# Performance work log

Hardware: AMD Instinct MI355X
Metric: run time of the kernel (lower is better)

## Reference

```python
import jax, jax.numpy as jnp
import numpy as np

N_NODES = 50000
N_EDGES = 800000
D_IN = 128
D_HID = 256
N_CLASSES = 2
N_GRAPHS = 256


def _graph_conv(x, src, dst, W_root, W_rel, b, num_nodes):
    # PyG GraphConv: out_i = W_root @ x_i + W_rel @ sum_{j->i} x_j + b
    agg = jax.ops.segment_sum(x[src], dst, num_segments=num_nodes)  # [N, d_in]
    return x @ W_root.T + agg @ W_rel.T + b


def setup_inputs() -> dict:
    key = jax.random.key(0)
    ks = jax.random.split(key, 12)
    x = jax.random.normal(ks[0], (N_NODES, D_IN), dtype=jnp.float32)
    edge_index = jax.random.randint(ks[1], (2, N_EDGES), 0, N_NODES, dtype=jnp.int64)
    batch = jnp.sort(jax.random.randint(ks[2], (N_NODES,), 0, N_GRAPHS, dtype=jnp.int64))
    s1 = 1.0 / np.sqrt(D_IN)
    s2 = 1.0 / np.sqrt(D_HID)
    W1_root = jax.random.uniform(ks[3], (D_HID, D_IN), minval=-s1, maxval=s1, dtype=jnp.float32)
    W1_rel = jax.random.uniform(ks[4], (D_HID, D_IN), minval=-s1, maxval=s1, dtype=jnp.float32)
    b1 = jax.random.uniform(ks[5], (D_HID,), minval=-s1, maxval=s1, dtype=jnp.float32)
    W2_root = jax.random.uniform(ks[6], (D_HID, D_HID), minval=-s2, maxval=s2, dtype=jnp.float32)
    W2_rel = jax.random.uniform(ks[7], (D_HID, D_HID), minval=-s2, maxval=s2, dtype=jnp.float32)
    b2 = jax.random.uniform(ks[8], (D_HID,), minval=-s2, maxval=s2, dtype=jnp.float32)
    Wfc = jax.random.uniform(ks[9], (N_CLASSES, D_HID), minval=-s2, maxval=s2, dtype=jnp.float32)
    bfc = jax.random.uniform(ks[10], (N_CLASSES,), minval=-s2, maxval=s2, dtype=jnp.float32)
    return {"x": x, "edge_index": edge_index, "batch": batch, "num_graphs": N_GRAPHS,
            "W1_root": W1_root, "W1_rel": W1_rel, "b1": b1,
            "W2_root": W2_root, "W2_rel": W2_rel, "b2": b2,
            "Wfc": Wfc, "bfc": bfc}


def reference(x, edge_index, batch, num_graphs, W1_root, W1_rel, b1, W2_root, W2_rel, b2, Wfc, bfc):
    src, dst = edge_index[0], edge_index[1]
    n = x.shape[0]
    h = jax.nn.relu(_graph_conv(x, src, dst, W1_root, W1_rel, b1, n))
    h = jax.nn.relu(_graph_conv(h, src, dst, W2_root, W2_rel, b2, n))
    # global mean pool over graph segments
    sums = jax.ops.segment_sum(h, batch, num_segments=num_graphs)        # [G, d]
    counts = jax.ops.segment_sum(jnp.ones((n,), h.dtype), batch, num_segments=num_graphs)
    pooled = sums / jnp.maximum(counts, 1.0)[:, None]
    logits = pooled @ Wfc.T + bfc
    return jax.nn.sigmoid(logits)
```

## Files before the change

### kernel.cpp

```cpp
#include <hip/hip_runtime.h>
#include <math.h>

#define D_IN 128
#define D_HID 256
#define N_CLASSES 2
#define N_GRAPHS 256
#define BUCKET 64

#define PSZ  256
#define NP   196
#define CAP  4608
#define LCAP 64
#define EPB  4096
#define PBT  1024

typedef __attribute__((ext_vector_type(8))) short short8;
typedef __attribute__((ext_vector_type(4))) float float4v;

__device__ __forceinline__ unsigned short f2bf(float f) {
    union { float f; unsigned int u; } v; v.f = f;
    unsigned int r = v.u + 0x7FFFu + ((v.u >> 16) & 1u);
    return (unsigned short)(r >> 16);
}
__device__ __forceinline__ float bf2f(unsigned short h) {
    union { unsigned int u; float f; } v; v.u = ((unsigned int)h) << 16;
    return v.f;
}

#define GLD_LDS16(gp, lp) __builtin_amdgcn_global_load_lds( \
    (const __attribute__((address_space(1))) void*)(gp),    \
    (__attribute__((address_space(3))) void*)(lp), 16, 0, 0)

__global__ void prep_kernel(const int* __restrict__ src, const int* __restrict__ dst,
                            int E, int nba,
                            int* __restrict__ pcnt, unsigned int* __restrict__ part,
                            const float* __restrict__ x,
                            const float* __restrict__ w1r, const float* __restrict__ w1a,
                            const float* __restrict__ w2r, const float* __restrict__ w2a,
                            unsigned short* __restrict__ xb,
                            unsigned short* __restrict__ o1r, unsigned short* __restrict__ o1a,
                            unsigned short* __restrict__ o2r, unsigned short* __restrict__ o2a,
                            int n4x) {
    __shared__ int lcnt[NP];
    __shared__ int lbase[NP];
    __shared__ unsigned int stage[NP][LCAP];

    const int tid = threadIdx.x;

    if (blockIdx.x >= nba) {
        int i = (blockIdx.x - nba) * PBT + tid;
        const float* in; unsigned short* out; int off;
        if (i < n4x)                 { in = x;   out = xb;  off = i; }
        else {
            int j = i - n4x;
            if (j < 8192)            { in = w1r; out = o1r; off = j; }
            else if (j < 16384)      { in = w1a; out = o1a; off = j - 8192; }
            else if (j < 32768)      { in = w2r; out = o2r; off = j - 16384; }
            else if (j < 49152)      { in = w2a; out = o2a; off = j - 32768; }
            else return;
        }
        float4 v = ((const float4*)in)[off];
        ushort4 o;
        o.x = f2bf(v.x); o.y = f2bf(v.y); o.z = f2bf(v.z); o.w = f2bf(v.w);
        ((ushort4*)out)[off] = o;
        return;
    }

    for (int p = tid; p < NP; p += PBT) lcnt[p] = 0;
    __syncthreads();

    const int e0 = blockIdx.x * EPB;
    const int e1 = min(E, e0 + EPB);
    for (int e = e0 + tid; e < e1; e += PBT) {
        int s = src[e];
        int d = dst[e];
        int p = d >> 8;
        unsigned int v = ((unsigned int)(d & (PSZ - 1)) << 16) | (unsigned int)s;
        int pos = atomicAdd(&lcnt[p], 1);
        if (pos < LCAP) stage[p][pos] = v;
        else {
            int g = atomicAdd(&pcnt[p], 1);
            if (g < CAP) part[(size_t)p * CAP + g] = v;
        }
    }
    __syncthreads();

    for (int p = tid; p < NP; p += PBT) {
        int nn = min(lcnt[p], LCAP);
        lbase[p] = atomicAdd(&pcnt[p], nn);
    }
    __syncthreads();

    const int wv = tid >> 6, lane = tid & 63;
    for (int p = wv; p < NP; p += PBT / 64) {
        const int nn = min(lcnt[p], LCAP);
        const int b = lbase[p];
        for (int i = lane; i < nn; i += 64) {
            int g = b + i;
            if (g < CAP) part[(size_t)p * CAP + g] = stage[p][i];
        }
    }
}

__global__ void bucket_kernel(const unsigned int* __restrict__ part,
                              const int* __restrict__ pcnt,
                              int* __restrict__ cursor,
                              unsigned short* __restrict__ srcs, int N) {
    __shared__ int lcur[PSZ];
    __shared__ __align__(16) unsigned short lsrc[PSZ][BUCKET];

    const int p = blockIdx.x;
    const int tid = threadIdx.x;

    if (tid < PSZ) lcur[tid] = 0;
    __syncthreads();

    const int n = min(pcnt[p], CAP);
    const unsigned int* pp = part + (size_t)p * CAP;
    for (int i = tid; i < n; i += PBT) {
        unsigned int v = pp[i];
        int dl = v >> 16;
        int pos = atomicAdd(&lcur[dl], 1);
        if (pos < BUCKET) lsrc[dl][pos] = (unsigned short)(v & 0xFFFFu);
    }
    __syncthreads();

    const int nodeBase = p * PSZ;
    if (tid < PSZ && nodeBase + tid < N) cursor[nodeBase + tid] = lcur[tid];

    const uint4* ls = (const uint4*)&lsrc[0][0];
    uint4* gs = (uint4*)(srcs + (size_t)nodeBase * BUCKET);
#pragma unroll
    for (int i = tid; i < PSZ * BUCKET / 8; i += PBT) {
        if (nodeBase + (i >> 3) < N) gs[i] = ls[i];
    }
}

template <int D>
__global__ void gather_bucket_bf16(const unsigned short* __restrict__ feat,
                                   const unsigned short* __restrict__ srcs,
                                   const int* __restrict__ cnt,
                                   unsigned short* __restrict__ agg, int N) {
    const int wave = (blockIdx.x * blockDim.x + threadIdx.x) >> 6;
    const int lane = threadIdx.x & 63;
    if (wave >= N) return;
    const unsigned short* bucket = srcs + (size_t)wave * BUCKET;
    int my = bucket[lane];
    const int c = min(cnt[wave], BUCKET);

    if (D == 256) {
        float a0 = 0.f, a1 = 0.f, a2 = 0.f, a3 = 0.f;
        float b0 = 0.f, b1 = 0.f, b2 = 0.f, b3 = 0.f;
        const unsigned short* base = feat + lane * 4;
        int i = 0;
        for (; i + 4 <= c; i += 4) {
            int s0 = __shfl(my, i + 0);
            int s1 = __shfl(my, i + 1);
            int s2 = __shfl(my, i + 2);
            int s3 = __shfl(my, i + 3);
            uint2 w0 = *(const uint2*)(base + (size_t)s0 * 256);
            uint2 w1 = *(const uint2*)(base + (size_t)s1 * 256);
            uint2 w2 = *(const uint2*)(base + (size_t)s2 * 256);
            uint2 w3 = *(const uint2*)(base + (size_t)s3 * 256);
            a0 += bf2f((unsigned short)(w0.x & 0xFFFF)); a1 += bf2f((unsigned short)(w0.x >> 16));
            a2 += bf2f((unsigned short)(w0.y & 0xFFFF)); a3 += bf2f((unsigned short)(w0.y >> 16));
            b0 += bf2f((unsigned short)(w1.x & 0xFFFF)); b1 += bf2f((unsigned short)(w1.x >> 16));
            b2 += bf2f((unsigned short)(w1.y & 0xFFFF)); b3 += bf2f((unsigned short)(w1.y >> 16));
            a0 += bf2f((unsigned short)(w2.x & 0xFFFF)); a1 += bf2f((unsigned short)(w2.x >> 16));
            a2 += bf2f((unsigned short)(w2.y & 0xFFFF)); a3 += bf2f((unsigned short)(w2.y >> 16));
            b0 += bf2f((unsigned short)(w3.x & 0xFFFF)); b1 += bf2f((unsigned short)(w3.x >> 16));
            b2 += bf2f((unsigned short)(w3.y & 0xFFFF)); b3 += bf2f((unsigned short)(w3.y >> 16));
        }
        for (; i < c; i++) {
            int s = __shfl(my, i);
            uint2 w = *(const uint2*)(base + (size_t)s * 256);
            a0 += bf2f((unsigned short)(w.x & 0xFFFF)); a1 += bf2f((unsigned short)(w.x >> 16));
            a2 += bf2f((unsigned short)(w.y & 0xFFFF)); a3 += bf2f((unsigned short)(w.y >> 16));
        }
        a0 += b0; a1 += b1; a2 += b2; a3 += b3;
        uint2 o;
        o.x = (unsigned int)f2bf(a0) | ((unsigned int)f2bf(a1) << 16);
        o.y = (unsigned int)f2bf(a2) | ((unsigned int)f2bf(a3) << 16);
        *(uint2*)(agg + (size_t)wave * 256 + lane * 4) = o;
    } else {
        const int half = lane >> 5;
        const int hl = lane & 31;
        float a0 = 0.f, a1 = 0.f, a2 = 0.f, a3 = 0.f;
        float b0 = 0.f, b1 = 0.f, b2 = 0.f, b3 = 0.f;
        const unsigned short* base = feat + hl * 4;
        int i = 0;
        for (; i + 4 <= c; i += 4) {
            int sA = __shfl(my, i + half);
            int sB = __shfl(my, i + 2 + half);
            uint2 wA = *(const uint2*)(base + (size_t)sA * 128);
            uint2 wB = *(const uint2*)(base + (size_t)sB * 128);
            a0 += bf2f((unsigned short)(wA.x & 0xFFFF)); a1 += bf2f((unsigned short)(wA.x >> 16));
            a2 += bf2f((unsigned short)(wA.y & 0xFFFF)); a3 += bf2f((unsigned short)(wA.y >> 16));
            b0 += bf2f((unsigned short)(wB.x & 0xFFFF)); b1 += bf2f((unsigned short)(wB.x >> 16));
            b2 += bf2f((unsigned short)(wB.y & 0xFFFF)); b3 += bf2f((unsigned short)(wB.y >> 16));
        }
        for (; i < c; i += 2) {
            if (i + half < c) {
                int s = __shfl(my, i + half);
                uint2 w = *(const uint2*)(base + (size_t)s * 128);
                a0 += bf2f((unsigned short)(w.x & 0xFFFF)); a1 += bf2f((unsigned short)(w.x >> 16));
                a2 += bf2f((unsigned short)(w.y & 0xFFFF)); a3 += bf2f((unsigned short)(w.y >> 16));
            }
        }
        a0 += b0; a1 += b1; a2 += b2; a3 += b3;
        a0 += __shfl_xor(a0, 32);
        a1 += __shfl_xor(a1, 32);
        a2 += __shfl_xor(a2, 32);
        a3 += __shfl_xor(a3, 32);
        if (half == 0) {
            uint2 o;
            o.x = (unsigned int)f2bf(a0) | ((unsigned int)f2bf(a1) << 16);
            o.y = (unsigned int)f2bf(a2) | ((unsigned int)f2bf(a3) << 16);
            *(uint2*)(agg + (size_t)wave * 128 + hl * 4) = o;
        }
    }
}

template <int K1>
__global__ void gemm_mfma_dual(const unsigned short* __restrict__ X,
                               const unsigned short* __restrict__ Ag,
                               const unsigned short* __restrict__ Wr,
                               const unsigned short* __restrict__ Wa,
                               const float* __restrict__ bias,
                               unsigned short* __restrict__ out,
                               int Nrows) {
    __shared__ __align__(16) unsigned short As[128][64];
    __shared__ __align__(16) unsigned short Bs[256][64];

    const int tid = threadIdx.x;
    const int w = tid >> 6;
    const int lane = tid & 63;
    const int quad = lane >> 4;
    const int r16 = lane & 15;
    const int sr8 = lane >> 3;
    const int sg  = lane & 7;
    const int sgs = sg ^ sr8;
    const int i0 = blockIdx.x * 128;
    const int m0 = (w >> 2) * 64;
    const int n0 = (w & 3) * 64;

    float4v acc[4][4];
#pragma unroll
    for (int mt = 0; mt < 4; mt++)
#pragma unroll
        for (int nt = 0; nt < 4; nt++) {
            float4v z = {0.f, 0.f, 0.f, 0.f};
            acc[mt][nt] = z;
        }

    for (int k0 = 0; k0 < 2 * K1; k0 += 64) {
        const bool first = (k0 < K1);
        const int kb = first ? k0 : (k0 - K1);
        const unsigned short* PA = first ? X : Ag;
        const unsigned short* PB = first ? Wr : Wa;

#pragma unroll
        for (int t = 0; t < 2; t++) {
            const int rr = w * 16 + t * 8;
            GLD_LDS16(PA + (size_t)(i0 + rr + sr8) * K1 + kb + sgs * 8, &As[rr][0]);
        }
#pragma unroll
        for (int t = 0; t < 4; t++) {
            const int rr = w * 32 + t * 8;
            GLD_LDS16(PB + (size_t)(rr + sr8) * K1 + kb + sgs * 8, &Bs[rr][0]);
        }
        __syncthreads();

#pragma unroll
        for (int ks = 0; ks < 2; ks++) {
            short8 af[4], bfr[4];
            const int pgq = ((ks * 4 + quad) ^ (r16 & 7)) * 8;
#pragma unroll
            for (int mt = 0; mt < 4; mt++)
                af[mt] = *(const short8*)&As[m0 + mt * 16 + r16][pgq];
#pragma unroll
            for (int nt = 0; nt < 4; nt++)
                bfr[nt] = *(const short8*)&Bs[n0 + nt * 16 + r16][pgq];
#pragma unroll
            for (int mt = 0; mt < 4; mt++)
#pragma unroll
                for (int nt = 0; nt < 4; nt++)
                    acc[mt][nt] = __builtin_amdgcn_mfma_f32_16x16x32_bf16(
                        af[mt], bfr[nt], acc[mt][nt], 0, 0, 0);
        }
        __syncthreads();
    }

#pragma unroll
    for (int mt = 0; mt < 4; mt++) {
#pragma unroll
        for (int e = 0; e < 4; e++) {
            const int m = i0 + m0 + mt * 16 + quad * 4 + e;
            if (m >= Nrows) continue;
#pragma unroll
            for (int nt = 0; nt < 4; nt++) {
                const int n = n0 + nt * 16 + r16;
                float v = acc[mt][nt][e] + bias[n];
                out[(size_t)m * 256 + n] = f2bf(fmaxf(v, 0.f));
            }
        }
    }
}

__global__ void pool_fc_kernel(const unsigned short* __restrict__ h,
                               const int* __restrict__ batch,
                               const float* __restrict__ Wfc,
                               const float* __restrict__ bfc,
                               float* __restrict__ out,
                               int N) {
    const int g = blockIdx.x;
    const int tid = threadIdx.x;
    const int wv = tid >> 6;
    const int lane = tid & 63;

    int lo = 0, hi = N;
    while (lo < hi) { int mid = (lo + hi) >> 1; if (batch[mid] < g) lo = mid + 1; else hi = mid; }
    const int start = lo;
    hi = N;
    while (lo < hi) { int mid = (lo + hi) >> 1; if (batch[mid] < g + 1) lo = mid + 1; else hi = mid; }
    const int end = lo;

    float a0 = 0.f, a1 = 0.f, a2 = 0.f, a3 = 0.f;
    float b0 = 0.f, b1 = 0.f, b2 = 0.f, b3 = 0.f;
    const unsigned short* base = h + lane * 4;
    int r = start + wv;
    for (; r + 16 < end; r += 32) {
        uint2 wA = *(const uint2*)(base + (size_t)r * 256);
        uint2 wB = *(const uint2*)(base + (size_t)(r + 16) * 256);
        a0 += bf2f((unsigned short)(wA.x & 0xFFFF)); a1 += bf2f((unsigned short)(wA.x >> 16));
        a2 += bf2f((unsigned short)(wA.y & 0xFFFF)); a3 += bf2f((unsigned short)(wA.y >> 16));
        b0 += bf2f((unsigned short)(wB.x & 0xFFFF)); b1 += bf2f((unsigned short)(wB.x >> 16));
        b2 += bf2f((unsigned short)(wB.y & 0xFFFF)); b3 += bf2f((unsigned short)(wB.y >> 16));
    }
    if (r < end) {
        uint2 wA = *(const uint2*)(base + (size_t)r * 256);
        a0 += bf2f((unsigned short)(wA.x & 0xFFFF)); a1 += bf2f((unsigned short)(wA.x >> 16));
        a2 += bf2f((unsigned short)(wA.y & 0xFFFF)); a3 += bf2f((unsigned short)(wA.y >> 16));
    }
    a0 += b0; a1 += b1; a2 += b2; a3 += b3;

    __shared__ float part[16][D_HID];
    part[wv][lane * 4 + 0] = a0;
    part[wv][lane * 4 + 1] = a1;
    part[wv][lane * 4 + 2] = a2;
    part[wv][lane * 4 + 3] = a3;
    __syncthreads();

    __shared__ float pooled[D_HID];
    __shared__ float red[2 * D_HID];
    if (tid < D_HID) {
        float s = 0.f;
#pragma unroll
        for (int w2 = 0; w2 < 16; w2++) s += part[w2][tid];
        const float cnt = fmaxf((float)(end - start), 1.0f);
        pooled[tid] = s / cnt;
    }
    __syncthreads();

    if (tid < 2 * D_HID) {
        const int c = tid >> 8;
        const int col = tid & 255;
        red[tid] = pooled[col] * Wfc[c * D_HID + col];
    }
    __syncthreads();
    for (int off = D_HID / 2; off > 0; off >>= 1) {
        if (tid < 2 * D_HID && (tid & 255) < off) red[tid] += red[tid + off];
        __syncthreads();
    }
    if (tid < N_CLASSES) {
        float logit = red[tid << 8] + bfc[tid];
        out[g * N_CLASSES + tid] = 1.0f / (1.0f + expf(-logit));
    }
}

extern "C" void kernel_launch(void* const* d_in, const int* in_sizes, int n_in,
                              void* d_out, int out_size, void* d_ws, size_t ws_size,
                              hipStream_t stream) {
    const float* x     = (const float*)d_in[0];
    const int*   edge  = (const int*)d_in[1];
    const int*   batch = (const int*)d_in[2];
    const float* W1r = (const float*)d_in[4];
    const float* W1a = (const float*)d_in[5];
    const float* b1  = (const float*)d_in[6];
    const float* W2r = (const float*)d_in[7];
    const float* W2a = (const float*)d_in[8];
    const float* b2  = (const float*)d_in[9];
    const float* Wfc = (const float*)d_in[10];
    const float* bfc = (const float*)d_in[11];

    const int N = in_sizes[0] / D_IN;
    const int E = in_sizes[1] / 2;
    const int* src = edge;
    const int* dst = edge + E;

    unsigned short* xb    = (unsigned short*)d_ws;
    unsigned short* agg1b = xb    + (size_t)N * 128;
    unsigned short* h1b   = agg1b + (size_t)N * 128;
    unsigned short* agg2b = h1b   + (size_t)N * 256;
    unsigned short* h2b   = agg2b + (size_t)N * 256;
    unsigned short* w1r_b = h2b   + (size_t)N * 256;
    unsigned short* w1a_b = w1r_b + 256 * 128;
    unsigned short* w2r_b = w1a_b + 256 * 128;
    unsigned short* w2a_b = w2r_b + 256 * 256;
    int* cursor = (int*)(w2a_b + 256 * 256);
    unsigned short* srcs = (unsigned short*)(cursor + N);
    int* pcnt = (int*)(srcs + (size_t)N * BUCKET);

    unsigned int* part = (unsigned int*)h2b;

    hipMemsetAsync(pcnt, 0, NP * sizeof(int), stream);

    const int nba = (E + EPB - 1) / EPB;
    const int n4x = N * D_IN / 4;
    const int cvtBlocks = (n4x + 49152 + PBT - 1) / PBT;
    prep_kernel<<<nba + cvtBlocks, PBT, 0, stream>>>(
        src, dst, E, nba, pcnt, part,
        x, W1r, W1a, W2r, W2a, xb, w1r_b, w1a_b, w2r_b, w2a_b, n4x);

    bucket_kernel<<<NP, PBT, 0, stream>>>(part, pcnt, cursor, srcs, N);

    gather_bucket_bf16<D_IN><<<(N + 3) / 4, 256, 0, stream>>>(xb, srcs, cursor, agg1b, N);
    gemm_mfma_dual<D_IN><<<(N + 127) / 128, 512, 0, stream>>>(
        xb, agg1b, w1r_b, w1a_b, b1, h1b, N);

    gather_bucket_bf16<D_HID><<<(N + 3) / 4, 256, 0, stream>>>(h1b, srcs, cursor, agg2b, N);
    gemm_mfma_dual<D_HID><<<(N + 127) / 128, 512, 0, stream>>>(
        h1b, agg2b, w2r_b, w2a_b, b2, h2b, N);

    pool_fc_kernel<<<N_GRAPHS, 1024, 0, stream>>>(h2b, batch, Wfc, bfc, (float*)d_out, N);
}
```

Measured before the change: 232.7 us.

## Split neighbor gather across eight feature slices per node

Each node's aggregation is now done by eight waves instead of one. Each wave owns a feature slice (32 columns for D=256, 16 for D=128), and its lane groups walk different neighbors in parallel before a cross-lane shuffle reduction. The goal is more memory-level parallelism, with many neighbor rows in flight per wave. The cost is eight times more blocks, redundant reads of the bucket and count per slice, and per-lane accesses of only 64-byte segments, which may waste cache-line bandwidth.

Result: slower. 385.4 us (+65.6%).

```diff
diff --git a/kernel.cpp b/kernel.cpp
--- a/kernel.cpp
+++ b/kernel.cpp
@@ -137,11 +137,12 @@
 }
 
 template <int D>
-__global__ void gather_bucket_bf16(const unsigned short* __restrict__ feat,
+__global__ void gather_sliced_bf16(const unsigned short* __restrict__ feat,
                                    const unsigned short* __restrict__ srcs,
                                    const int* __restrict__ cnt,
                                    unsigned short* __restrict__ agg, int N) {
-    const int wave = (blockIdx.x * blockDim.x + threadIdx.x) >> 6;
+    const int slice = blockIdx.x & 7;
+    const int wave = (blockIdx.x >> 3) * (blockDim.x >> 6) + (threadIdx.x >> 6);
     const int lane = threadIdx.x & 63;
     if (wave >= N) return;
     const unsigned short* bucket = srcs + (size_t)wave * BUCKET;
@@ -149,74 +150,56 @@
     const int c = min(cnt[wave], BUCKET);
 
     if (D == 256) {
+        const int g = lane >> 3;
+        const int p = lane & 7;
         float a0 = 0.f, a1 = 0.f, a2 = 0.f, a3 = 0.f;
-        float b0 = 0.f, b1 = 0.f, b2 = 0.f, b3 = 0.f;
-        const unsigned short* base = feat + lane * 4;
-        int i = 0;
-        for (; i + 4 <= c; i += 4) {
-            int s0 = __shfl(my, i + 0);
-            int s1 = __shfl(my, i + 1);
-            int s2 = __shfl(my, i + 2);
-            int s3 = __shfl(my, i + 3);
-            uint2 w0 = *(const uint2*)(base + (size_t)s0 * 256);
-            uint2 w1 = *(const uint2*)(base + (size_t)s1 * 256);
-            uint2 w2 = *(const uint2*)(base + (size_t)s2 * 256);
-            uint2 w3 = *(const uint2*)(base + (size_t)s3 * 256);
-            a0 += bf2f((unsigned short)(w0.x & 0xFFFF)); a1 += bf2f((unsigned short)(w0.x >> 16));
-            a2 += bf2f((unsigned short)(w0.y & 0xFFFF)); a3 += bf2f((unsigned short)(w0.y >> 16));
-            b0 += bf2f((unsigned short)(w1.x & 0xFFFF)); b1 += bf2f((unsigned short)(w1.x >> 16));
-            b2 += bf2f((unsigned short)(w1.y & 0xFFFF)); b3 += bf2f((unsigned short)(w1.y >> 16));
-            a0 += bf2f((unsigned short)(w2.x & 0xFFFF)); a1 += bf2f((unsigned short)(w2.x >> 16));
-            a2 += bf2f((unsigned short)(w2.y & 0xFFFF)); a3 += bf2f((unsigned short)(w2.y >> 16));
-            b0 += bf2f((unsigned short)(w3.x & 0xFFFF)); b1 += bf2f((unsigned short)(w3.x >> 16));
-            b2 += bf2f((unsigned short)(w3.y & 0xFFFF)); b3 += bf2f((unsigned short)(w3.y >> 16));
-        }
-        for (; i < c; i++) {
-            int s = __shfl(my, i);
-            uint2 w = *(const uint2*)(base + (size_t)s * 256);
-            a0 += bf2f((unsigned short)(w.x & 0xFFFF)); a1 += bf2f((unsigned short)(w.x >> 16));
-            a2 += bf2f((unsigned short)(w.y & 0xFFFF)); a3 += bf2f((unsigned short)(w.y >> 16));
-        }
-        a0 += b0; a1 += b1; a2 += b2; a3 += b3;
-        uint2 o;
-        o.x = (unsigned int)f2bf(a0) | ((unsigned int)f2bf(a1) << 16);
-        o.y = (unsigned int)f2bf(a2) | ((unsigned int)f2bf(a3) << 16);
-        *(uint2*)(agg + (size_t)wave * 256 + lane * 4) = o;
+        const unsigned short* base = feat + slice * 32 + p * 4;
+        for (int i = 0; i < c; i += 8) {
+            if (i + g < c) {
+                int s = __shfl(my, i + g);
+                uint2 w = *(const uint2*)(base + (size_t)s * 256);
+                a0 += bf2f((unsigned short)(w.x & 0xFFFF)); a1 += bf2f((unsigned short)(w.x >> 16));
+                a2 += bf2f((unsigned short)(w.y & 0xFFFF)); a3 += bf2f((unsigned short)(w.y >> 16));
+            }
+        }
+#pragma unroll
+        for (int st = 8; st < 64; st <<= 1) {
+            a0 += __shfl_xor(a0, st);
+            a1 += __shfl_xor(a1, st);
+            a2 += __shfl_xor(a2, st);
+            a3 += __shfl_xor(a3, st);
+        }
+        if (g == 0) {
+            uint2 o;
+            o.x = (unsigned int)f2bf(a0) | ((unsigned int)f2bf(a1) << 16);
+            o.y = (unsigned int)f2bf(a2) | ((unsigned int)f2bf(a3) << 16);
+            *(uint2*)(agg + (size_t)wave * 256 + slice * 32 + p * 4) = o;
+        }
     } else {
-        const int half = lane >> 5;
-        const int hl = lane & 31;
+        const int g = lane >> 2;
+        const int p = lane & 3;
         float a0 = 0.f, a1 = 0.f, a2 = 0.f, a3 = 0.f;
-        float b0 = 0.f, b1 = 0.f, b2 = 0.f, b3 = 0.f;
-        const unsigned short* base = feat + hl * 4;
-        int i = 0;
-        for (; i + 4 <= c; i += 4) {
-            int sA = __shfl(my, i + half);
-            int sB = __shfl(my, i + 2 + half);
-            uint2 wA = *(const uint2*)(base + (size_t)sA * 128);
-            uint2 wB = *(const uint2*)(base + (size_t)sB * 128);
-            a0 += bf2f((unsigned short)(wA.x & 0xFFFF)); a1 += bf2f((unsigned short)(wA.x >> 16));
-            a2 += bf2f((unsigned short)(wA.y & 0xFFFF)); a3 += bf2f((unsigned short)(wA.y >> 16));
-            b0 += bf2f((unsigned short)(wB.x & 0xFFFF)); b1 += bf2f((unsigned short)(wB.x >> 16));
-            b2 += bf2f((unsigned short)(wB.y & 0xFFFF)); b3 += bf2f((unsigned short)(wB.y >> 16));
-        }
-        for (; i < c; i += 2) {
-            if (i + half < c) {
-                int s = __shfl(my, i + half);
+        const unsigned short* base = feat + slice * 16 + p * 4;
+        for (int i = 0; i < c; i += 16) {
+            if (i + g < c) {
+                int s = __shfl(my, i + g);
                 uint2 w = *(const uint2*)(base + (size_t)s * 128);
                 a0 += bf2f((unsigned short)(w.x & 0xFFFF)); a1 += bf2f((unsigned short)(w.x >> 16));
                 a2 += bf2f((unsigned short)(w.y & 0xFFFF)); a3 += bf2f((unsigned short)(w.y >> 16));
             }
         }
-        a0 += b0; a1 += b1; a2 += b2; a3 += b3;
-        a0 += __shfl_xor(a0, 32);
-        a1 += __shfl_xor(a1, 32);
-        a2 += __shfl_xor(a2, 32);
-        a3 += __shfl_xor(a3, 32);
-        if (half == 0) {
+#pragma unroll
+        for (int st = 4; st < 64; st <<= 1) {
+            a0 += __shfl_xor(a0, st);
+            a1 += __shfl_xor(a1, st);
+            a2 += __shfl_xor(a2, st);
+            a3 += __shfl_xor(a3, st);
+        }
+        if (g == 0) {
             uint2 o;
             o.x = (unsigned int)f2bf(a0) | ((unsigned int)f2bf(a1) << 16);
             o.y = (unsigned int)f2bf(a2) | ((unsigned int)f2bf(a3) << 16);
-            *(uint2*)(agg + (size_t)wave * 128 + hl * 4) = o;
+            *(uint2*)(agg + (size_t)wave * 128 + slice * 16 + p * 4) = o;
         }
     }
 }
@@ -424,11 +407,12 @@
 
     bucket_kernel<<<NP, PBT, 0, stream>>>(part, pcnt, cursor, srcs, N);
 
-    gather_bucket_bf16<D_IN><<<(N + 3) / 4, 256, 0, stream>>>(xb, srcs, cursor, agg1b, N);
+    const int ngrp = (N + 3) / 4;
+    gather_sliced_bf16<D_IN><<<ngrp * 8, 256, 0, stream>>>(xb, srcs, cursor, agg1b, N);
     gemm_mfma_dual<D_IN><<<(N + 127) / 128, 512, 0, stream>>>(
         xb, agg1b, w1r_b, w1a_b, b1, h1b, N);
 
-    gather_bucket_bf16<D_HID><<<(N + 3) / 4, 256, 0, stream>>>(h1b, srcs, cursor, agg2b, N);
+    gather_sliced_bf16<D_HID><<<ngrp * 8, 256, 0, stream>>>(h1b, srcs, cursor, agg2b, N);
     gemm_mfma_dual<D_HID><<<(N + 127) / 128, 512, 0, stream>>>(
         h1b, agg2b, w2r_b, w2a_b, b2, h2b, N);
 
```
